# Performance work log

Hardware: AMD Instinct MI355X
Metric: run time of the kernel (lower is better)

## Reference

```python
import jax, jax.numpy as jnp
import numpy as np

N = 100000       # nodes
E = 1200000      # edges
D_IN = 64
D_OUT = 64
ALPHA = 0.01     # LeakyReLU negative slope
EPS = 1e-5       # BatchNorm eps


def setup_inputs() -> dict:
    key = jax.random.key(0)
    k0, k1, k2, k3 = jax.random.split(key, 4)
    x = jax.random.normal(k0, (N, D_IN), dtype=jnp.float32)
    edge_idx = jax.random.randint(k1, (2, E), 0, N)
    edge_attr = jax.random.uniform(k2, (E,), dtype=jnp.float32)
    W = jax.random.normal(k3, (D_IN, D_OUT), dtype=jnp.float32) * (1.0 / np.sqrt(D_IN))
    b = jnp.zeros((D_OUT,), dtype=jnp.float32)
    gamma = jnp.ones((D_OUT,), dtype=jnp.float32)
    beta = jnp.zeros((D_OUT,), dtype=jnp.float32)
    return {"x": x, "edge_idx": edge_idx, "edge_attr": edge_attr,
            "W": W, "b": b, "gamma": gamma, "beta": beta}


def reference(x, edge_idx, edge_attr, W, b, gamma, beta):
    n = x.shape[0]
    row, col = edge_idx[0], edge_idx[1]
    # --- GCNConv: add self-loops, symmetric normalization ---
    loops = jnp.arange(n)
    row_f = jnp.concatenate([row, loops])                       # [E+N]
    col_f = jnp.concatenate([col, loops])                       # [E+N]
    w_f = jnp.concatenate([edge_attr, jnp.ones((n,), x.dtype)])  # [E+N]
    deg = jax.ops.segment_sum(w_f, col_f, num_segments=n)       # [N]
    deg_safe = jnp.where(deg > 0, deg, 1.0)
    dis = jnp.where(deg > 0, jax.lax.rsqrt(deg_safe), 0.0)      # deg^-1/2
    norm = dis[row_f] * w_f * dis[col_f]                        # [E+N]
    h = x @ W                                                   # [N, D_OUT]
    msg = norm[:, None] * h[row_f]                              # gather + scale
    agg = jax.ops.segment_sum(msg, col_f, num_segments=n) + b   # scatter-add
    # --- BatchNorm (training-mode batch stats, biased var) ---
    mean = jnp.mean(agg, axis=0)
    var = jnp.mean((agg - mean) ** 2, axis=0)
    hn = (agg - mean) * jax.lax.rsqrt(var + EPS) * gamma + beta
    # --- LeakyReLU ---
    return jnp.where(hn >= 0, hn, ALPHA * hn)
```

## Files before the change

kernel.cpp:

```cpp
#include <hip/hip_runtime.h>

#define D 64
#define ALPHA 0.01f
#define EPS 1e-5f
#define NREP 8
#define CAP 48
#define GSZ 128
#define GMAX 1024
#define NB 256

typedef __attribute__((ext_vector_type(8))) short short8;
typedef __attribute__((ext_vector_type(4))) float f32x4;

__device__ inline unsigned short f2bf(float f) {
    unsigned u = __float_as_uint(f);
    u += 0x7fffu + ((u >> 16) & 1u);
    return (unsigned short)(u >> 16);
}
__device__ inline float bf2f(unsigned short h) { return __uint_as_float((unsigned)h << 16); }

__global__ __launch_bounds__(256) void k_prepA(const float4* __restrict__ x4,
                                               ushort4* __restrict__ xb4,
                                               float* __restrict__ stats,
                                               const int* __restrict__ col,
                                               int* __restrict__ cnt_gb,
                                               long long n16, int G, int E) {
    __shared__ int h[GMAX];
    if (blockIdx.x < NB) {
        int b = blockIdx.x;
        for (int i = threadIdx.x; i < G; i += 256) h[i] = 0;
        __syncthreads();
        int chunk = (E + NB - 1) / NB;
        int e0 = b * chunk;
        int e1 = e0 + chunk; if (e1 > E) e1 = E;
        for (int e = e0 + threadIdx.x; e < e1; e += 256)
            atomicAdd(&h[col[e] >> 7], 1);
        __syncthreads();
        for (int i = threadIdx.x; i < G; i += 256)
            cnt_gb[i * NB + b] = h[i];
    } else {
        long long i = (long long)(blockIdx.x - NB) * 256 + threadIdx.x;
        if (i < n16) {
            float4 v = x4[i];
            ushort4 r;
            r.x = f2bf(v.x); r.y = f2bf(v.y); r.z = f2bf(v.z); r.w = f2bf(v.w);
            xb4[i] = r;
        }
        if (i < NREP * 128) stats[i] = 0.0f;
    }
}

__global__ __launch_bounds__(256) void k_scanA(const int* __restrict__ cnt_gb,
                                               int* __restrict__ bsum, int M) {
    __shared__ int ls[256];
    int base = blockIdx.x * 1024 + threadIdx.x * 4;
    int s = 0;
    if (base + 3 < M) {
        int4 v = *(const int4*)&cnt_gb[base];
        s = v.x + v.y + v.z + v.w;
    } else {
#pragma unroll
        for (int k = 0; k < 4; ++k) { int idx = base + k; if (idx < M) s += cnt_gb[idx]; }
    }
    ls[threadIdx.x] = s;
    __syncthreads();
    for (int off = 128; off > 0; off >>= 1) {
        if (threadIdx.x < off) ls[threadIdx.x] += ls[threadIdx.x + off];
        __syncthreads();
    }
    if (threadIdx.x == 0) bsum[blockIdx.x] = ls[0];
}

__global__ __launch_bounds__(256) void k_scanC(const int* __restrict__ cnt_gb,
                                               const int* __restrict__ bsum,
                                               int* __restrict__ pos,
                                               int* __restrict__ gseg, int M, int G, int E) {
    __shared__ int ls[256];
    int t = threadIdx.x;
    ls[t] = (t < blockIdx.x) ? bsum[t] : 0;
    __syncthreads();
    for (int off = 128; off > 0; off >>= 1) {
        if (t < off) ls[t] += ls[t + off];
        __syncthreads();
    }
    int base_total = ls[0];
    __syncthreads();
    int base = blockIdx.x * 1024 + t * 4;
    int v[4];
    int s = 0;
#pragma unroll
    for (int k = 0; k < 4; ++k) { int idx = base + k; v[k] = (idx < M) ? cnt_gb[idx] : 0; s += v[k]; }
    ls[t] = s;
    __syncthreads();
    int own = s;
    for (int off = 1; off < 256; off <<= 1) {
        int tv = (t >= off) ? ls[t - off] : 0;
        __syncthreads();
        ls[t] += tv;
        __syncthreads();
    }
    int excl = ls[t] - own + base_total;
#pragma unroll
    for (int k = 0; k < 4; ++k) {
        int idx = base + k;
        if (idx < M) {
            pos[idx] = excl;
            if ((idx & (NB - 1)) == 0) gseg[idx >> 8] = excl;
        }
        excl += v[k];
    }
    if (blockIdx.x == 0 && t == 0) gseg[G] = E;
}

__global__ __launch_bounds__(256) void k_binB(const int* __restrict__ eidx,
                                              const float* __restrict__ w,
                                              const int* __restrict__ pos,
                                              uint2* __restrict__ seg, int G, int E) {
    __shared__ int cursor[GMAX];
    int b = blockIdx.x;
    for (int g = threadIdx.x; g < G; g += 256) cursor[g] = pos[g * NB + b];
    __syncthreads();
    int chunk = (E + NB - 1) / NB;
    int e0 = b * chunk;
    int e1 = e0 + chunk; if (e1 > E) e1 = E;
    for (int e = e0 + threadIdx.x; e < e1; e += 256) {
        int row = eidx[e];
        int c = eidx[E + e];
        unsigned wq = (unsigned)(w[e] * 32767.0f + 0.5f);
        int slot = atomicAdd(&cursor[c >> 7], 1);
        seg[slot] = make_uint2((wq << 17) | (unsigned)row, (unsigned)(c & (GSZ - 1)));
    }
}

__global__ __launch_bounds__(256) void k_binC(const uint2* __restrict__ seg,
                                              const int* __restrict__ gseg,
                                              unsigned* __restrict__ bucket,
                                              int* __restrict__ cnt,
                                              float* __restrict__ dis,
                                              float* __restrict__ dis_s, int n) {
    __shared__ int cl[GSZ];
    __shared__ float ws[GSZ];
    int g = blockIdx.x;
    if (threadIdx.x < GSZ) { cl[threadIdx.x] = 0; ws[threadIdx.x] = 0.0f; }
    __syncthreads();
    int s0 = gseg[g], s1 = gseg[g + 1];
    for (int i = s0 + threadIdx.x; i < s1; i += 256) {
        uint2 ev = seg[i];
        int cig = (int)ev.y;
        int rank = atomicAdd(&cl[cig], 1);
        atomicAdd(&ws[cig], (float)(ev.x >> 17) * (1.0f / 32767.0f));
        int node = g * GSZ + cig;
        if (rank < CAP) bucket[(size_t)node * CAP + rank] = ev.x;
    }
    __syncthreads();
    if (threadIdx.x < GSZ) {
        int node = g * GSZ + threadIdx.x;
        if (node < n) {
            cnt[node] = cl[threadIdx.x];
            float d = rsqrtf(1.0f + ws[threadIdx.x]);
            dis[node] = d;
            dis_s[node] = d * (1.0f / 32767.0f);
        }
    }
}

__global__ __launch_bounds__(256) void k_gather(const unsigned short* __restrict__ xb,
                                                const unsigned* __restrict__ bucket,
                                                const int* __restrict__ cnt,
                                                const float* __restrict__ dis,
                                                const float* __restrict__ dis_s,
                                                unsigned short* __restrict__ aggb, int n) {
    int node = blockIdx.x * 4 + (threadIdx.x >> 6);
    if (node >= n) return;
    int lane = threadIdx.x & 63;
    int g = lane >> 3;
    int l = lane & 7;
    int c = cnt[node];
    if (c > CAP) c = CAP;
    float di = dis[node];
    float acc[8] = {0, 0, 0, 0, 0, 0, 0, 0};
    if (g == 0) {
        short8 xv = *(const short8*)(xb + ((size_t)node << 6) + l * 8);
#pragma unroll
        for (int k = 0; k < 8; ++k) acc[k] = bf2f((unsigned short)xv[k]) * di;
    }
    const unsigned* bkt = bucket + (size_t)node * CAP;
    int j0 = g, j1 = g + 8;
    unsigned v0 = (j0 < c) ? bkt[j0] : 0u;
    unsigned v1 = (j1 < c) ? bkt[j1] : 0u;
    while (j0 < c) {
        int p0 = j0 + 16, p1 = j1 + 16;
        unsigned w0 = (p0 < c) ? bkt[p0] : 0u;
        unsigned w1 = (p1 < c) ? bkt[p1] : 0u;
        int s0 = (int)(v0 & 0x1FFFFu);
        int s1 = (int)(v1 & 0x1FFFFu);
        float nr0 = (float)(v0 >> 17) * dis_s[s0];
        float nr1 = (float)(v1 >> 17) * dis_s[s1];
        short8 x0 = *(const short8*)(xb + ((size_t)s0 << 6) + l * 8);
        short8 x1 = *(const short8*)(xb + ((size_t)s1 << 6) + l * 8);
#pragma unroll
        for (int k = 0; k < 8; ++k) acc[k] += nr0 * bf2f((unsigned short)x0[k]);
#pragma unroll
        for (int k = 0; k < 8; ++k) acc[k] += nr1 * bf2f((unsigned short)x1[k]);
        v0 = w0; v1 = w1; j0 = p0; j1 = p1;
    }
#pragma unroll
    for (int off = 8; off <= 32; off <<= 1)
#pragma unroll
        for (int k = 0; k < 8; ++k) acc[k] += __shfl_xor(acc[k], off, 64);
    if (g == 0) {
        short8 r;
#pragma unroll
        for (int k = 0; k < 8; ++k) r[k] = (short)f2bf(acc[k] * di);
        *(short8*)(aggb + ((size_t)node << 6) + l * 8) = r;
    }
}

__global__ __launch_bounds__(256) void k_gemmstats(const unsigned short* __restrict__ aggb,
                                                   const float* __restrict__ Wm,
                                                   float* __restrict__ out,
                                                   float* __restrict__ stats, int n) {
    __shared__ unsigned short Wt[64 * 64];
    __shared__ float ssum[4][64], qsum[4][64];
    int tid = threadIdx.x;
    for (int i = tid; i < 4096; i += 256) {
        int k = i >> 6, nn = i & 63;
        Wt[nn * 64 + k] = f2bf(Wm[i]);
    }
    __syncthreads();
    int wv = tid >> 6;
    int lane = tid & 63;
    int l15 = lane & 15;
    int quad = lane >> 4;

    short8 bfrag[2][4];
#pragma unroll
    for (int h = 0; h < 2; ++h)
#pragma unroll
        for (int g = 0; g < 4; ++g)
            bfrag[h][g] = *(const short8*)&Wt[(g * 16 + l15) * 64 + h * 32 + quad * 8];

    float s[4] = {0, 0, 0, 0}, q[4] = {0, 0, 0, 0};
    int nwt = (n + 15) >> 4;
    for (int wt = blockIdx.x * 4 + wv; wt < nwt; wt += gridDim.x * 4) {
        int row0 = wt * 16;
        int arow = row0 + l15;
        if (arow >= n) arow = n - 1;
        const unsigned short* ap = aggb + (size_t)arow * 64 + quad * 8;
        short8 a0 = *(const short8*)ap;
        short8 a1 = *(const short8*)(ap + 32);
        f32x4 acc[4] = {{0, 0, 0, 0}, {0, 0, 0, 0}, {0, 0, 0, 0}, {0, 0, 0, 0}};
#pragma unroll
        for (int g = 0; g < 4; ++g) {
            acc[g] = __builtin_amdgcn_mfma_f32_16x16x32_bf16(a0, bfrag[0][g], acc[g], 0, 0, 0);
            acc[g] = __builtin_amdgcn_mfma_f32_16x16x32_bf16(a1, bfrag[1][g], acc[g], 0, 0, 0);
        }
#pragma unroll
        for (int r = 0; r < 4; ++r) {
            int row = row0 + quad * 4 + r;
            if (row < n) {
                size_t base = (size_t)row * 64;
#pragma unroll
                for (int g = 0; g < 4; ++g) {
                    float v = acc[g][r];
                    out[base + g * 16 + l15] = v;
                    s[g] += v;
                    q[g] += v * v;
                }
            }
        }
    }
#pragma unroll
    for (int off = 16; off <= 32; off <<= 1) {
#pragma unroll
        for (int g = 0; g < 4; ++g) {
            s[g] += __shfl_xor(s[g], off, 64);
            q[g] += __shfl_xor(q[g], off, 64);
        }
    }
    if (quad == 0) {
#pragma unroll
        for (int g = 0; g < 4; ++g) { ssum[wv][g * 16 + l15] = s[g]; qsum[wv][g * 16 + l15] = q[g]; }
    }
    __syncthreads();
    float* st = stats + (blockIdx.x & (NREP - 1)) * 128;
    if (tid < 64)
        atomicAdd(&st[tid], ssum[0][tid] + ssum[1][tid] + ssum[2][tid] + ssum[3][tid]);
    else if (tid < 128) {
        int t = tid - 64;
        atomicAdd(&st[64 + t], qsum[0][t] + qsum[1][t] + qsum[2][t] + qsum[3][t]);
    }
}

__global__ __launch_bounds__(256) void k_norm(float4* __restrict__ out4,
                                              const float* __restrict__ stats,
                                              const float* __restrict__ gamma,
                                              const float* __restrict__ beta, int n) {
    __shared__ float scale[64], shift[64];
    if (threadIdx.x < 64) {
        float sm = 0.0f, qm = 0.0f;
#pragma unroll
        for (int r = 0; r < NREP; ++r) {
            sm += stats[r * 128 + threadIdx.x];
            qm += stats[r * 128 + 64 + threadIdx.x];
        }
        float inv_n = 1.0f / (float)n;
        float mean = sm * inv_n;
        float var = qm * inv_n - mean * mean;
        float sc = rsqrtf(var + EPS) * gamma[threadIdx.x];
        scale[threadIdx.x] = sc;
        shift[threadIdx.x] = beta[threadIdx.x] - mean * sc;
    }
    __syncthreads();
    long long idx = (long long)blockIdx.x * blockDim.x + threadIdx.x;
    if (idx < (long long)n * 16) {
        int l = (int)(idx & 15);
        float4 v = out4[idx];
        float4 r;
        float a, b2;
        a = scale[l * 4 + 0]; b2 = shift[l * 4 + 0]; r.x = v.x * a + b2; r.x = r.x >= 0.0f ? r.x : ALPHA * r.x;
        a = scale[l * 4 + 1]; b2 = shift[l * 4 + 1]; r.y = v.y * a + b2; r.y = r.y >= 0.0f ? r.y : ALPHA * r.y;
        a = scale[l * 4 + 2]; b2 = shift[l * 4 + 2]; r.z = v.z * a + b2; r.z = r.z >= 0.0f ? r.z : ALPHA * r.z;
        a = scale[l * 4 + 3]; b2 = shift[l * 4 + 3]; r.w = v.w * a + b2; r.w = r.w >= 0.0f ? r.w : ALPHA * r.w;
        out4[idx] = r;
    }
}

extern "C" void kernel_launch(void* const* d_in, const int* in_sizes, int n_in,
                              void* d_out, int out_size, void* d_ws, size_t ws_size,
                              hipStream_t stream) {
    const float* x     = (const float*)d_in[0];
    const int*   eidx  = (const int*)d_in[1];
    const float* eattr = (const float*)d_in[2];
    const float* Wm    = (const float*)d_in[3];
    const float* gamma = (const float*)d_in[5];
    const float* beta  = (const float*)d_in[6];
    float* out = (float*)d_out;

    int n = in_sizes[0] / D;
    int E = in_sizes[2];
    int G = (n + GSZ - 1) / GSZ;
    int M = G * NB;
    int nbs = (M + 1023) / 1024;

    char* p = (char*)d_ws;
    uint2* seg = (uint2*)p;                     p += (size_t)E * 8;
    unsigned* bucket = (unsigned*)p;            p += (size_t)n * CAP * 4;
    unsigned short* xb   = (unsigned short*)p;  p += (size_t)n * D * 2;
    unsigned short* aggb = (unsigned short*)p;  p += (size_t)n * D * 2;
    int* cnt = (int*)p;                         p += (size_t)n * 4;
    float* dis = (float*)p;                     p += (size_t)n * 4;
    float* dis_s = (float*)p;                   p += (size_t)n * 4;
    float* stats = (float*)p;                   p += NREP * 128 * 4;
    int* cnt_gb = (int*)p;                      p += (size_t)M * 4;
    int* pos = (int*)p;                         p += (size_t)M * 4;
    int* gseg = (int*)p;                        p += ((size_t)G + 1) * 4;
    int* bsum = (int*)p;                        p += 256 * 4;

    long long n16 = (long long)n * 16;
    unsigned prep_blocks = (unsigned)((n16 + 255) / 256);

    k_prepA<<<NB + prep_blocks, 256, 0, stream>>>(
        (const float4*)x, (ushort4*)xb, stats, eidx + E, cnt_gb, n16, G, E);
    k_scanA<<<nbs, 256, 0, stream>>>(cnt_gb, bsum, M);
    k_scanC<<<nbs, 256, 0, stream>>>(cnt_gb, bsum, pos, gseg, M, G, E);
    k_binB<<<NB, 256, 0, stream>>>(eidx, eattr, pos, seg, G, E);
    k_binC<<<G, 256, 0, stream>>>(seg, gseg, bucket, cnt, dis, dis_s, n);
    k_gather<<<(n + 3) / 4, 256, 0, stream>>>(xb, bucket, cnt, dis, dis_s, aggb, n);
    k_gemmstats<<<1024, 256, 0, stream>>>(aggb, Wm, out, stats, n);
    k_norm<<<(unsigned)((n16 + 255) / 256), 256, 0, stream>>>(
        (float4*)out, stats, gamma, beta, n);
}
```

Baseline: 185.6 us.

## Fuse neighbor gather with MFMA GEMM and stats via LDS tile

Merges the gather/aggregate kernel and the GEMM+statistics kernel into one persistent kernel. Each wave aggregates 16 nodes into an LDS tile, then runs the bf16 MFMA on that tile and accumulates BatchNorm sums. This removes the aggb round trip through global memory and one launch. In exchange, parallelism drops from one wave per node across about 25k blocks to a fixed 1024-block grid with sequential per-node loops, and block-wide barriers are added, so gather latency hiding may be worse.

```diff
diff --git a/kernel.cpp b/kernel.cpp
--- a/kernel.cpp
+++ b/kernel.cpp
@@ -8,6 +8,7 @@
 #define GSZ 128
 #define GMAX 1024
 #define NB 256
+#define GMS 72
 
 typedef __attribute__((ext_vector_type(8))) short short8;
 typedef __attribute__((ext_vector_type(4))) float f32x4;
@@ -164,63 +165,16 @@
     }
 }
 
-__global__ __launch_bounds__(256) void k_gather(const unsigned short* __restrict__ xb,
-                                                const unsigned* __restrict__ bucket,
-                                                const int* __restrict__ cnt,
-                                                const float* __restrict__ dis,
-                                                const float* __restrict__ dis_s,
-                                                unsigned short* __restrict__ aggb, int n) {
-    int node = blockIdx.x * 4 + (threadIdx.x >> 6);
-    if (node >= n) return;
-    int lane = threadIdx.x & 63;
-    int g = lane >> 3;
-    int l = lane & 7;
-    int c = cnt[node];
-    if (c > CAP) c = CAP;
-    float di = dis[node];
-    float acc[8] = {0, 0, 0, 0, 0, 0, 0, 0};
-    if (g == 0) {
-        short8 xv = *(const short8*)(xb + ((size_t)node << 6) + l * 8);
-#pragma unroll
-        for (int k = 0; k < 8; ++k) acc[k] = bf2f((unsigned short)xv[k]) * di;
-    }
-    const unsigned* bkt = bucket + (size_t)node * CAP;
-    int j0 = g, j1 = g + 8;
-    unsigned v0 = (j0 < c) ? bkt[j0] : 0u;
-    unsigned v1 = (j1 < c) ? bkt[j1] : 0u;
-    while (j0 < c) {
-        int p0 = j0 + 16, p1 = j1 + 16;
-        unsigned w0 = (p0 < c) ? bkt[p0] : 0u;
-        unsigned w1 = (p1 < c) ? bkt[p1] : 0u;
-        int s0 = (int)(v0 & 0x1FFFFu);
-        int s1 = (int)(v1 & 0x1FFFFu);
-        float nr0 = (float)(v0 >> 17) * dis_s[s0];
-        float nr1 = (float)(v1 >> 17) * dis_s[s1];
-        short8 x0 = *(const short8*)(xb + ((size_t)s0 << 6) + l * 8);
-        short8 x1 = *(const short8*)(xb + ((size_t)s1 << 6) + l * 8);
-#pragma unroll
-        for (int k = 0; k < 8; ++k) acc[k] += nr0 * bf2f((unsigned short)x0[k]);
-#pragma unroll
-        for (int k = 0; k < 8; ++k) acc[k] += nr1 * bf2f((unsigned short)x1[k]);
-        v0 = w0; v1 = w1; j0 = p0; j1 = p1;
-    }
-#pragma unroll
-    for (int off = 8; off <= 32; off <<= 1)
-#pragma unroll
-        for (int k = 0; k < 8; ++k) acc[k] += __shfl_xor(acc[k], off, 64);
-    if (g == 0) {
-        short8 r;
-#pragma unroll
-        for (int k = 0; k < 8; ++k) r[k] = (short)f2bf(acc[k] * di);
-        *(short8*)(aggb + ((size_t)node << 6) + l * 8) = r;
-    }
-}
-
-__global__ __launch_bounds__(256) void k_gemmstats(const unsigned short* __restrict__ aggb,
-                                                   const float* __restrict__ Wm,
-                                                   float* __restrict__ out,
-                                                   float* __restrict__ stats, int n) {
+__global__ __launch_bounds__(256) void k_gathermm(const unsigned short* __restrict__ xb,
+                                                  const unsigned* __restrict__ bucket,
+                                                  const int* __restrict__ cnt,
+                                                  const float* __restrict__ dis,
+                                                  const float* __restrict__ dis_s,
+                                                  const float* __restrict__ Wm,
+                                                  float* __restrict__ out,
+                                                  float* __restrict__ stats, int n) {
     __shared__ unsigned short Wt[64 * 64];
+    __shared__ unsigned short tileA[4][16 * GMS];
     __shared__ float ssum[4][64], qsum[4][64];
     int tid = threadIdx.x;
     for (int i = tid; i < 4096; i += 256) {
@@ -230,57 +184,116 @@
     __syncthreads();
     int wv = tid >> 6;
     int lane = tid & 63;
+    int g = lane >> 3;
+    int l = lane & 7;
     int l15 = lane & 15;
     int quad = lane >> 4;
-
-    short8 bfrag[2][4];
-#pragma unroll
-    for (int h = 0; h < 2; ++h)
-#pragma unroll
-        for (int g = 0; g < 4; ++g)
-            bfrag[h][g] = *(const short8*)&Wt[(g * 16 + l15) * 64 + h * 32 + quad * 8];
+    unsigned short* tA = tileA[wv];
 
     float s[4] = {0, 0, 0, 0}, q[4] = {0, 0, 0, 0};
     int nwt = (n + 15) >> 4;
-    for (int wt = blockIdx.x * 4 + wv; wt < nwt; wt += gridDim.x * 4) {
+    int stride = gridDim.x * 4;
+    int base_wt = blockIdx.x * 4 + wv;
+    int iters = 0;
+    {
+        int first = blockIdx.x * 4;
+        if (first < nwt) iters = (nwt - first + stride - 1) / stride;
+    }
+    for (int it = 0; it < iters; ++it) {
+        int wt = base_wt + it * stride;
+        bool wvalid = wt < nwt;
         int row0 = wt * 16;
-        int arow = row0 + l15;
-        if (arow >= n) arow = n - 1;
-        const unsigned short* ap = aggb + (size_t)arow * 64 + quad * 8;
-        short8 a0 = *(const short8*)ap;
-        short8 a1 = *(const short8*)(ap + 32);
-        f32x4 acc[4] = {{0, 0, 0, 0}, {0, 0, 0, 0}, {0, 0, 0, 0}, {0, 0, 0, 0}};
-#pragma unroll
-        for (int g = 0; g < 4; ++g) {
-            acc[g] = __builtin_amdgcn_mfma_f32_16x16x32_bf16(a0, bfrag[0][g], acc[g], 0, 0, 0);
-            acc[g] = __builtin_amdgcn_mfma_f32_16x16x32_bf16(a1, bfrag[1][g], acc[g], 0, 0, 0);
-        }
-#pragma unroll
-        for (int r = 0; r < 4; ++r) {
-            int row = row0 + quad * 4 + r;
-            if (row < n) {
-                size_t base = (size_t)row * 64;
-#pragma unroll
-                for (int g = 0; g < 4; ++g) {
-                    float v = acc[g][r];
-                    out[base + g * 16 + l15] = v;
-                    s[g] += v;
-                    q[g] += v * v;
+        if (wvalid) {
+            for (int i = 0; i < 16; ++i) {
+                int node = row0 + i;
+                float acc[8] = {0, 0, 0, 0, 0, 0, 0, 0};
+                float di = 0.0f;
+                if (node < n) {
+                    int c = cnt[node];
+                    if (c > CAP) c = CAP;
+                    di = dis[node];
+                    if (g == 0) {
+                        short8 xv = *(const short8*)(xb + ((size_t)node << 6) + l * 8);
+#pragma unroll
+                        for (int k = 0; k < 8; ++k) acc[k] = bf2f((unsigned short)xv[k]) * di;
+                    }
+                    const unsigned* bkt = bucket + (size_t)node * CAP;
+                    int j0 = g, j1 = g + 8;
+                    unsigned v0 = (j0 < c) ? bkt[j0] : 0u;
+                    unsigned v1 = (j1 < c) ? bkt[j1] : 0u;
+                    while (j0 < c) {
+                        int p0 = j0 + 16, p1 = j1 + 16;
+                        unsigned w0 = (p0 < c) ? bkt[p0] : 0u;
+                        unsigned w1 = (p1 < c) ? bkt[p1] : 0u;
+                        int s0 = (int)(v0 & 0x1FFFFu);
+                        int s1 = (int)(v1 & 0x1FFFFu);
+                        float nr0 = (float)(v0 >> 17) * dis_s[s0];
+                        float nr1 = (float)(v1 >> 17) * dis_s[s1];
+                        short8 x0 = *(const short8*)(xb + ((size_t)s0 << 6) + l * 8);
+                        short8 x1 = *(const short8*)(xb + ((size_t)s1 << 6) + l * 8);
+#pragma unroll
+                        for (int k = 0; k < 8; ++k) acc[k] += nr0 * bf2f((unsigned short)x0[k]);
+#pragma unroll
+                        for (int k = 0; k < 8; ++k) acc[k] += nr1 * bf2f((unsigned short)x1[k]);
+                        v0 = w0; v1 = w1; j0 = p0; j1 = p1;
+                    }
+#pragma unroll
+                    for (int off = 8; off <= 32; off <<= 1)
+#pragma unroll
+                        for (int k = 0; k < 8; ++k) acc[k] += __shfl_xor(acc[k], off, 64);
+                }
+                if (g == 0) {
+                    short8 r;
+#pragma unroll
+                    for (int k = 0; k < 8; ++k) r[k] = (short)f2bf(acc[k] * di);
+                    *(short8*)&tA[i * GMS + l * 8] = r;
                 }
             }
         }
+        __syncthreads();
+        if (wvalid) {
+            short8 bfrag[2][4];
+#pragma unroll
+            for (int h = 0; h < 2; ++h)
+#pragma unroll
+                for (int gg = 0; gg < 4; ++gg)
+                    bfrag[h][gg] = *(const short8*)&Wt[(gg * 16 + l15) * 64 + h * 32 + quad * 8];
+            short8 a0 = *(const short8*)&tA[l15 * GMS + quad * 8];
+            short8 a1 = *(const short8*)&tA[l15 * GMS + 32 + quad * 8];
+            f32x4 accC[4] = {{0, 0, 0, 0}, {0, 0, 0, 0}, {0, 0, 0, 0}, {0, 0, 0, 0}};
+#pragma unroll
+            for (int gg = 0; gg < 4; ++gg) {
+                accC[gg] = __builtin_amdgcn_mfma_f32_16x16x32_bf16(a0, bfrag[0][gg], accC[gg], 0, 0, 0);
+                accC[gg] = __builtin_amdgcn_mfma_f32_16x16x32_bf16(a1, bfrag[1][gg], accC[gg], 0, 0, 0);
+            }
+#pragma unroll
+            for (int r = 0; r < 4; ++r) {
+                int row = row0 + quad * 4 + r;
+                if (row < n) {
+                    size_t base = (size_t)row * 64;
+#pragma unroll
+                    for (int gg = 0; gg < 4; ++gg) {
+                        float v = accC[gg][r];
+                        out[base + gg * 16 + l15] = v;
+                        s[gg] += v;
+                        q[gg] += v * v;
+                    }
+                }
+            }
+        }
+        __syncthreads();
     }
 #pragma unroll
     for (int off = 16; off <= 32; off <<= 1) {
 #pragma unroll
-        for (int g = 0; g < 4; ++g) {
-            s[g] += __shfl_xor(s[g], off, 64);
-            q[g] += __shfl_xor(q[g], off, 64);
+        for (int gg = 0; gg < 4; ++gg) {
+            s[gg] += __shfl_xor(s[gg], off, 64);
+            q[gg] += __shfl_xor(q[gg], off, 64);
         }
     }
     if (quad == 0) {
 #pragma unroll
-        for (int g = 0; g < 4; ++g) { ssum[wv][g * 16 + l15] = s[g]; qsum[wv][g * 16 + l15] = q[g]; }
+        for (int gg = 0; gg < 4; ++gg) { ssum[wv][gg * 16 + l15] = s[gg]; qsum[wv][gg * 16 + l15] = q[gg]; }
     }
     __syncthreads();
     float* st = stats + (blockIdx.x & (NREP - 1)) * 128;
@@ -347,7 +360,6 @@
     uint2* seg = (uint2*)p;                     p += (size_t)E * 8;
     unsigned* bucket = (unsigned*)p;            p += (size_t)n * CAP * 4;
     unsigned short* xb   = (unsigned short*)p;  p += (size_t)n * D * 2;
-    unsigned short* aggb = (unsigned short*)p;  p += (size_t)n * D * 2;
     int* cnt = (int*)p;                         p += (size_t)n * 4;
     float* dis = (float*)p;                     p += (size_t)n * 4;
     float* dis_s = (float*)p;                   p += (size_t)n * 4;
@@ -366,8 +378,7 @@
     k_scanC<<<nbs, 256, 0, stream>>>(cnt_gb, bsum, pos, gseg, M, G, E);
     k_binB<<<NB, 256, 0, stream>>>(eidx, eattr, pos, seg, G, E);
     k_binC<<<G, 256, 0, stream>>>(seg, gseg, bucket, cnt, dis, dis_s, n);
-    k_gather<<<(n + 3) / 4, 256, 0, stream>>>(xb, bucket, cnt, dis, dis_s, aggb, n);
-    k_gemmstats<<<1024, 256, 0, stream>>>(aggb, Wm, out, stats, n);
+    k_gathermm<<<1024, 256, 0, stream>>>(xb, bucket, cnt, dis, dis_s, Wm, out, stats, n);
     k_norm<<<(unsigned)((n16 + 255) / 256), 256, 0, stream>>>(
         (float4*)out, stats, gamma, beta, n);
 }
```

After: 215.1 us. +15.9%, slower.
